# Kernel optimization log

Hardware: AMD Instinct MI355X
Metric: run time of the kernel (lower is better)

The kernel has to match this reference:

```python
import jax, jax.numpy as jnp
import numpy as np
import math

NUM_HEADS = 16
VEC_SIZE = 1024
HEAD_DIM = VEC_SIZE // NUM_HEADS


def setup_inputs() -> dict:
    key = jax.random.key(0)
    k1, k2, k3, k4, k5 = jax.random.split(key, 5)
    B, S, D = 2, 2048, VEC_SIZE
    x = jax.random.normal(k1, (B, S, D), dtype=jnp.float32)
    # Linear params, torch-style: y = x @ W.T + b
    s1 = 1.0 / math.sqrt(D)
    W_qkv = jax.random.uniform(k2, (3 * D, D), minval=-s1, maxval=s1, dtype=jnp.float32)
    b_qkv = jax.random.uniform(k3, (3 * D,), minval=-s1, maxval=s1, dtype=jnp.float32)
    W_out = jax.random.uniform(k4, (D, D), minval=-s1, maxval=s1, dtype=jnp.float32)
    b_out = jax.random.uniform(k5, (D,), minval=-s1, maxval=s1, dtype=jnp.float32)
    return {"x": x, "W_qkv": W_qkv, "b_qkv": b_qkv, "W_out": W_out, "b_out": b_out}


def reference(x, W_qkv, b_qkv, W_out, b_out):
    B, S, D = x.shape
    H, Hd = NUM_HEADS, HEAD_DIM
    qkv = x @ W_qkv.T + b_qkv                      # [B,S,3D]
    q, k, v = jnp.split(qkv, 3, axis=-1)
    # [B,S,H,Hd] -> [B,H,S,Hd]
    q = q.reshape(B, S, H, Hd).transpose(0, 2, 1, 3)
    k = k.reshape(B, S, H, Hd).transpose(0, 2, 1, 3)
    v = v.reshape(B, S, H, Hd).transpose(0, 2, 1, 3)
    weight = jnp.einsum('bhqd,bhkd->bhqk', q, k)   # [B,H,S,S]
    causal = jnp.triu(jnp.ones((S, S), dtype=bool), k=1)
    weight = jnp.where(causal, -jnp.inf, weight)
    weight = weight / jnp.sqrt(jnp.asarray(Hd, dtype=weight.dtype))
    weight = jax.nn.softmax(weight, axis=-1)
    out = jnp.einsum('bhqk,bhkd->bhqd', weight, v)  # [B,H,S,Hd]
    out = out.transpose(0, 2, 1, 3).reshape(B, S, D)
    return out @ W_out.T + b_out
```

## Files before the change

kernel.cpp:

```cpp
#include <hip/hip_runtime.h>
#include <hip/hip_bf16.h>

typedef __attribute__((ext_vector_type(8))) short short8;
typedef __attribute__((ext_vector_type(4))) short s4v;
typedef __attribute__((ext_vector_type(4))) float floatx4;

__device__ inline floatx4 mfma_bf16(short8 a, short8 b, floatx4 c) {
  return __builtin_amdgcn_mfma_f32_16x16x32_bf16(a, b, c, 0, 0, 0);
}
__device__ inline float exp2_fast(float x) { return __builtin_amdgcn_exp2f(x); }

__device__ inline short bf16s(float f) {
  __hip_bfloat16 h = __float2bfloat16(f);
  return *reinterpret_cast<short*>(&h);
}
__device__ inline float sbf16(short s) {
  return __bfloat162float(*reinterpret_cast<__hip_bfloat16*>(&s));
}

__device__ inline void gld16(__hip_bfloat16* lds, const __hip_bfloat16* g) {
  __builtin_amdgcn_global_load_lds(
      (const __attribute__((address_space(1))) void*)g,
      (__attribute__((address_space(3))) void*)lds, 16, 0, 0);
}

__global__ __launch_bounds__(256) void cvt_all(
    const float* __restrict__ x, const float* __restrict__ wqkv,
    const float* __restrict__ wout, __hip_bfloat16* __restrict__ xb,
    __hip_bfloat16* __restrict__ wqkvb, __hip_bfloat16* __restrict__ wob) {
  const int n1 = 4194304, n2 = 3145728;
  int i = (blockIdx.x * 256 + threadIdx.x) * 8;
  const float* src;
  __hip_bfloat16* dst;
  int off;
  if (i < n1) { src = x; dst = xb; off = i; }
  else if (i < n1 + n2) { src = wqkv; dst = wqkvb; off = i - n1; }
  else { src = wout; dst = wob; off = i - n1 - n2; }
  float4 a = *reinterpret_cast<const float4*>(src + off);
  float4 b = *reinterpret_cast<const float4*>(src + off + 4);
  __hip_bfloat16 t[8];
  t[0] = __float2bfloat16(a.x); t[1] = __float2bfloat16(a.y);
  t[2] = __float2bfloat16(a.z); t[3] = __float2bfloat16(a.w);
  t[4] = __float2bfloat16(b.x); t[5] = __float2bfloat16(b.y);
  t[6] = __float2bfloat16(b.z); t[7] = __float2bfloat16(b.w);
  *reinterpret_cast<short8*>(dst + off) = *reinterpret_cast<short8*>(t);
}

__device__ inline void stage_half(__hip_bfloat16* lds, const __hip_bfloat16* g,
                                  int K, int tid) {
#pragma unroll
  for (int it = 0; it < 2; ++it) {
    int idx = it * 512 + tid;
    int row = idx >> 3, col = ((idx & 7) ^ (row & 7)) * 8;
    gld16(lds + idx * 8, g + (size_t)row * K + col);
  }
}
__device__ inline void stage_q(__hip_bfloat16* lds, const __hip_bfloat16* g,
                               int K, int tid) {
  int row = tid >> 3, col = ((tid & 7) ^ (row & 7)) * 8;
  gld16(lds + tid * 8, g + (size_t)row * K + col);
}

#define VMW(N) asm volatile("s_waitcnt vmcnt(" #N ")" ::: "memory")
#define BAR __builtin_amdgcn_s_barrier()

#define LDA8(dst, BUF, MH)                                                     \
  do {                                                                         \
    _Pragma("unroll") for (int mf = 0; mf < 4; ++mf) {                         \
      int rh = wm * 64 + mf * 16 + l15;                                        \
      _Pragma("unroll") for (int ks = 0; ks < 2; ++ks)                         \
          dst[mf][ks] = *reinterpret_cast<const short8*>(                      \
              &SA[BUF][MH][rh * 64 + (((ks * 4 + quad) ^ (rh & 7)) * 8)]);     \
    }                                                                          \
  } while (0)
#define LDB4(dst, BUF, NH)                                                     \
  do {                                                                         \
    _Pragma("unroll") for (int nf = 0; nf < 2; ++nf) {                         \
      int rh = wn * 32 + nf * 16 + l15;                                        \
      _Pragma("unroll") for (int ks = 0; ks < 2; ++ks)                         \
          dst[nf][ks] = *reinterpret_cast<const short8*>(                      \
              &SB[BUF][NH][rh * 64 + (((ks * 4 + quad) ^ (rh & 7)) * 8)]);     \
    }                                                                          \
  } while (0)
#define MM16(MH, NH, AF, BF)                                                   \
  do {                                                                         \
    _Pragma("unroll") for (int mf = 0; mf < 4; ++mf)                           \
        _Pragma("unroll") for (int nf = 0; nf < 2; ++nf) {                     \
      acc[MH][NH][mf][nf] = mfma_bf16(AF[mf][0], BF[nf][0], acc[MH][NH][mf][nf]); \
      acc[MH][NH][mf][nf] = mfma_bf16(AF[mf][1], BF[nf][1], acc[MH][NH][mf][nf]); \
    }                                                                          \
  } while (0)
#define PH(RD, STG, MH, NH, AF, BF, WT)                                        \
  do {                                                                         \
    RD;                                                                        \
    STG;                                                                       \
    __builtin_amdgcn_s_setprio(1);                                             \
    MM16(MH, NH, AF, BF);                                                      \
    __builtin_amdgcn_s_setprio(0);                                             \
    WT;                                                                        \
    BAR;                                                                       \
  } while (0)

template<bool OUT_BF16>
__global__ __launch_bounds__(512, 2) void gemm_256(
    const __hip_bfloat16* __restrict__ A, const __hip_bfloat16* __restrict__ Bt,
    const float* __restrict__ bias, void* __restrict__ Cout,
    int M, int N, int K) {
  __shared__ __align__(16) __hip_bfloat16 SA[2][2][128 * 64];
  __shared__ __align__(16) __hip_bfloat16 SB[2][2][128 * 64];
  const int tid = threadIdx.x;
  const int lane = tid & 63, quad = (lane >> 4), l15 = lane & 15;
  const int wave = tid >> 6;
  const int wm = wave >> 2, wn = wave & 3;

  const int nbx = gridDim.x;
  int bid = blockIdx.y * nbx + blockIdx.x;
  const int nwg = nbx * gridDim.y;
  if ((nwg & 7) == 0) bid = (bid & 7) * (nwg >> 3) + (bid >> 3);
  const int bx = bid % nbx, by = bid / nbx;
  const int m0 = by * 256, n0 = bx * 256;

  const __hip_bfloat16* Abase = A + (size_t)m0 * K;
  const __hip_bfloat16* Bbase = Bt + (size_t)n0 * K;
  const int NT = K >> 6;

  floatx4 acc[2][2][4][2];
#pragma unroll
  for (int a = 0; a < 2; ++a)
#pragma unroll
    for (int b = 0; b < 2; ++b)
#pragma unroll
      for (int c = 0; c < 4; ++c)
#pragma unroll
        for (int d = 0; d < 2; ++d) acc[a][b][c][d] = (floatx4){0.f, 0.f, 0.f, 0.f};

  short8 af0[4][2], af1[4][2];
  short8 bf0[2][2], bf1[2][2];

  stage_half(&SA[0][0][0], Abase, K, tid);
  stage_half(&SB[0][0][0], Bbase, K, tid);
  stage_half(&SA[0][1][0], Abase + (size_t)128 * K, K, tid);
  stage_half(&SB[0][1][0], Bbase + (size_t)128 * K, K, tid);
  stage_half(&SA[1][0][0], Abase + 64, K, tid);
  stage_half(&SB[1][0][0], Bbase + 64, K, tid);
  stage_half(&SA[1][1][0], Abase + (size_t)128 * K + 64, K, tid);
  stage_half(&SB[1][1][0], Bbase + (size_t)128 * K + 64, K, tid);
  VMW(12);
  BAR;

  for (int t = 0; t <= NT - 3; ++t) {
    const int cb = t & 1;
    const size_t k2 = (size_t)(t + 2) * 64;
    PH({ LDA8(af0, cb, 0); LDB4(bf0, cb, 0); }, (void)0,
       0, 0, af0, bf0, VMW(10));
    PH(LDA8(af1, cb, 1),
       { stage_half(&SA[cb][0][0], Abase + k2, K, tid);
         stage_half(&SB[cb][0][0], Bbase + k2, K, tid); },
       1, 0, af1, bf0, VMW(12));
    PH(LDB4(bf1, cb, 1),
       stage_half(&SA[cb][1][0], Abase + (size_t)128 * K + k2, K, tid),
       1, 1, af1, bf1, (void)0);
    PH((void)0,
       stage_half(&SB[cb][1][0], Bbase + (size_t)128 * K + k2, K, tid),
       0, 1, af0, bf1, VMW(12));
  }
  {
    const int cb = (NT - 2) & 1;
    PH({ LDA8(af0, cb, 0); LDB4(bf0, cb, 0); }, (void)0, 0, 0, af0, bf0, VMW(10));
    PH(LDA8(af1, cb, 1), (void)0, 1, 0, af1, bf0, VMW(8));
    PH(LDB4(bf1, cb, 1), (void)0, 1, 1, af1, bf1, (void)0);
    PH((void)0, (void)0, 0, 1, af0, bf1, VMW(4));
  }
  {
    const int cb = (NT - 1) & 1;
    PH({ LDA8(af0, cb, 0); LDB4(bf0, cb, 0); }, (void)0, 0, 0, af0, bf0, VMW(2));
    PH(LDA8(af1, cb, 1), (void)0, 1, 0, af1, bf0, VMW(0));
    LDB4(bf1, cb, 1);
    __builtin_amdgcn_s_setprio(1);
    MM16(1, 1, af1, bf1);
    MM16(0, 1, af0, bf1);
    __builtin_amdgcn_s_setprio(0);
  }

#pragma unroll
  for (int nh = 0; nh < 2; ++nh)
#pragma unroll
    for (int nf = 0; nf < 2; ++nf) {
      int gn = n0 + nh * 128 + wn * 32 + nf * 16 + l15;
      float bv = bias[gn];
#pragma unroll
      for (int mh = 0; mh < 2; ++mh)
#pragma unroll
        for (int mf = 0; mf < 4; ++mf)
#pragma unroll
          for (int rg = 0; rg < 4; ++rg) {
            int gm = m0 + mh * 128 + wm * 64 + mf * 16 + quad * 4 + rg;
            float v = acc[mh][nh][mf][nf][rg] + bv;
            if (OUT_BF16)
              ((__hip_bfloat16*)Cout)[(size_t)gm * N + gn] = __float2bfloat16(v);
            else
              ((float*)Cout)[(size_t)gm * N + gn] = v;
          }
    }
}

__global__ __launch_bounds__(512, 2) void gemm_n64(
    const __hip_bfloat16* __restrict__ A, const __hip_bfloat16* __restrict__ Bt,
    const float* __restrict__ bias, float* __restrict__ Cout,
    int M, int N, int K) {
  __shared__ __align__(16) __hip_bfloat16 SA[3][2][128 * 64];
  __shared__ __align__(16) __hip_bfloat16 SB[3][64 * 64];
  const int tid = threadIdx.x;
  const int lane = tid & 63, quad = (lane >> 4), l15 = lane & 15;
  const int wave = tid >> 6;
  const int wm = wave >> 2, wn = wave & 3;

  const int nbx = gridDim.x;
  int bid = blockIdx.y * nbx + blockIdx.x;
  const int nwg = nbx * gridDim.y;
  if ((nwg & 7) == 0) bid = (bid & 7) * (nwg >> 3) + (bid >> 3);
  const int bx = bid % nbx, by = bid / nbx;
  const int m0 = by * 256, n0 = bx * 64;

  const __hip_bfloat16* Abase = A + (size_t)m0 * K;
  const __hip_bfloat16* Bbase = Bt + (size_t)n0 * K;
  const int NT = K >> 6;

  floatx4 acc[2][4];
#pragma unroll
  for (int a = 0; a < 2; ++a)
#pragma unroll
    for (int c = 0; c < 4; ++c) acc[a][c] = (floatx4){0.f, 0.f, 0.f, 0.f};

  short8 af0[4][2], af1[4][2];
  short8 bf[2];

#define N64_LDA(dst, BUF, MH)                                                  \
  do {                                                                         \
    _Pragma("unroll") for (int mf = 0; mf < 4; ++mf) {                         \
      int rh = wm * 64 + mf * 16 + l15;                                        \
      _Pragma("unroll") for (int ks = 0; ks < 2; ++ks)                         \
          dst[mf][ks] = *reinterpret_cast<const short8*>(                      \
              &SA[BUF][MH][rh * 64 + (((ks * 4 + quad) ^ (rh & 7)) * 8)]);     \
    }                                                                          \
  } while (0)
#define N64_LDB(BUF)                                                           \
  do {                                                                         \
    int rh = wn * 16 + l15;                                                    \
    _Pragma("unroll") for (int ks = 0; ks < 2; ++ks)                           \
        bf[ks] = *reinterpret_cast<const short8*>(                             \
            &SB[BUF][rh * 64 + (((ks * 4 + quad) ^ (rh & 7)) * 8)]);           \
  } while (0)
#define N64_MM(MH, AF)                                                         \
  do {                                                                         \
    _Pragma("unroll") for (int mf = 0; mf < 4; ++mf) {                         \
      acc[MH][mf] = mfma_bf16(AF[mf][0], bf[0], acc[MH][mf]);                  \
      acc[MH][mf] = mfma_bf16(AF[mf][1], bf[1], acc[MH][mf]);                  \
    }                                                                          \
  } while (0)

  stage_half(&SA[0][0][0], Abase, K, tid);
  stage_half(&SA[0][1][0], Abase + (size_t)128 * K, K, tid);
  stage_q(&SB[0][0], Bbase, K, tid);
  stage_half(&SA[1][0][0], Abase + 64, K, tid);
  stage_half(&SA[1][1][0], Abase + (size_t)128 * K + 64, K, tid);
  stage_q(&SB[1][0], Bbase + 64, K, tid);
  VMW(5);
  BAR;

  int cb = 0, sb = 2;
  for (int t = 0; t <= NT - 3; ++t) {
    const size_t k2 = (size_t)(t + 2) * 64;
    N64_LDA(af0, cb, 0);
    N64_LDA(af1, cb, 1);
    N64_LDB(cb);
    stage_half(&SA[sb][0][0], Abase + k2, K, tid);
    stage_half(&SA[sb][1][0], Abase + (size_t)128 * K + k2, K, tid);
    stage_q(&SB[sb][0], Bbase + k2, K, tid);
    __builtin_amdgcn_s_setprio(1);
    N64_MM(0, af0);
    N64_MM(1, af1);
    __builtin_amdgcn_s_setprio(0);
    VMW(5);
    BAR;
    cb = (cb == 2) ? 0 : cb + 1;
    sb = (sb == 2) ? 0 : sb + 1;
  }
  {
    N64_LDA(af0, cb, 0);
    N64_LDA(af1, cb, 1);
    N64_LDB(cb);
    __builtin_amdgcn_s_setprio(1);
    N64_MM(0, af0);
    N64_MM(1, af1);
    __builtin_amdgcn_s_setprio(0);
    VMW(0);
    BAR;
    cb = (cb == 2) ? 0 : cb + 1;
  }
  {
    N64_LDA(af0, cb, 0);
    N64_LDA(af1, cb, 1);
    N64_LDB(cb);
    __builtin_amdgcn_s_setprio(1);
    N64_MM(0, af0);
    N64_MM(1, af1);
    __builtin_amdgcn_s_setprio(0);
  }

  {
    int gn = n0 + wn * 16 + l15;
    float bv = bias[gn];
#pragma unroll
    for (int mh = 0; mh < 2; ++mh)
#pragma unroll
      for (int mf = 0; mf < 4; ++mf)
#pragma unroll
        for (int rg = 0; rg < 4; ++rg) {
          int gm = m0 + mh * 128 + wm * 64 + mf * 16 + quad * 4 + rg;
          Cout[(size_t)gm * N + gn] = acc[mh][mf][rg] + bv;
        }
  }
#undef N64_LDA
#undef N64_LDB
#undef N64_MM
}

__global__ __launch_bounds__(256, 3) void flash_attn(
    const __hip_bfloat16* __restrict__ qkv, __hip_bfloat16* __restrict__ out) {
  const int S = 2048, QKV = 3072;
  const int bx = blockIdx.x;
  const int g = (blockIdx.y >> 3) + 2 * blockIdx.z;
  int qt;
  if (g == 0)      qt = bx;
  else if (g == 1) qt = 31 - bx;
  else if (g == 2) qt = (bx + 8) & 31;
  else             qt = (23 - bx) & 31;
  const int h = blockIdx.y, b = blockIdx.z;
  const int q0 = qt * 64;
  __shared__ __align__(16) short Ps[2][64 * 64];
  const int tid = threadIdx.x;
  const int wave = tid >> 6, lane = tid & 63, quad = lane >> 4, l15 = lane & 15;
  const int rx = l15 & 7;
  const __hip_bfloat16* base = qkv + (size_t)b * S * QKV;
  const float c2 = 0.18033688011112042f;
  const floatx4 zero4 = {0.f, 0.f, 0.f, 0.f};
  const int krow = 16 * wave + l15;

  const __hip_bfloat16* kbase = base + 1024 + h * 64;
  const __hip_bfloat16* vbase = base + 2048 + h * 64;

  for (int it = 0; it < 2; ++it) {
    int v = tid + it * 256;
    int row = v >> 3, cb = v & 7;
    int colp = (cb ^ (row & 7)) * 8;
    short8 qv = *reinterpret_cast<const short8*>(
        base + (size_t)(q0 + row) * QKV + h * 64 + cb * 8);
    short qs[8];
    for (int e = 0; e < 8; ++e) qs[e] = bf16s(sbf16(qv[e]) * c2);
    *reinterpret_cast<short8*>(&Ps[1][row * 64 + colp]) = *reinterpret_cast<short8*>(qs);
  }
  short8 kA0 = *reinterpret_cast<const short8*>(
      kbase + (size_t)krow * QKV + quad * 8);
  short8 kA1 = *reinterpret_cast<const short8*>(
      kbase + (size_t)krow * QKV + 32 + quad * 8);
  __syncthreads();

  short8 aq[4][2];
  for (int t4 = 0; t4 < 4; ++t4)
    for (int s = 0; s < 2; ++s)
      aq[t4][s] = *reinterpret_cast<const short8*>(
          &Ps[1][(t4 * 16 + l15) * 64 + (((s * 4 + quad) ^ rx) * 8)]);

  floatx4 o_acc[4];
  for (int m = 0; m < 4; ++m) o_acc[m] = zero4;
  float lsum4[4] = {0.f, 0.f, 0.f, 0.f};
  short8 vA0, vA1;

  for (int j = 0; j <= qt; ++j) {
    const int cj = j & 1, pj = cj ^ 1;

    short8 kB0, kB1, vB0, vB1;
    if (j < qt) {
      const __hip_bfloat16* kp = kbase + (size_t)((j + 1) * 64 + krow) * QKV;
      kB0 = *reinterpret_cast<const short8*>(kp + quad * 8);
      kB1 = *reinterpret_cast<const short8*>(kp + 32 + quad * 8);
    }
    {
      const __hip_bfloat16* vp = vbase + (size_t)(j * 64 + quad * 8) * QKV + krow;
      for (int i = 0; i < 8; ++i) {
        vB0[i] = *reinterpret_cast<const short*>(vp + (size_t)i * QKV);
        vB1[i] = *reinterpret_cast<const short*>(vp + (size_t)(32 + i) * QKV);
      }
    }

    if (j > 0) {
      for (int s = 0; s < 2; ++s) {
        short8 bv = s ? vA1 : vA0;
        for (int m = 0; m < 4; ++m) {
          short8 ap = *reinterpret_cast<const short8*>(
              &Ps[pj][(m * 16 + l15) * 64 + (((4 * s + quad) ^ rx) * 8)]);
          o_acc[m] = mfma_bf16(ap, bv, o_acc[m]);
        }
      }
    }

    floatx4 sc[4];
    for (int t4 = 0; t4 < 4; ++t4) {
      sc[t4] = mfma_bf16(kA0, aq[t4][0], zero4);
      sc[t4] = mfma_bf16(kA1, aq[t4][1], sc[t4]);
    }
    if (j == qt) {
      int kloc = 16 * wave + quad * 4;
      for (int t4 = 0; t4 < 4; ++t4)
        for (int rg = 0; rg < 4; ++rg)
          if (kloc + rg > t4 * 16 + l15) sc[t4][rg] = -1e30f;
    }

    const int pcol = ((2 * wave + (quad >> 1)) ^ rx) * 8 + (quad & 1) * 4;
    for (int t4 = 0; t4 < 4; ++t4) {
      short pp[4];
      for (int rg = 0; rg < 4; ++rg) {
        float p = exp2_fast(sc[t4][rg]);
        lsum4[t4] += p;
        pp[rg] = bf16s(p);
      }
      *reinterpret_cast<s4v*>(&Ps[cj][(t4 * 16 + l15) * 64 + pcol]) =
          *reinterpret_cast<s4v*>(pp);
    }

    kA0 = kB0; kA1 = kB1; vA0 = vB0; vA1 = vB1;
    __syncthreads();
  }

  const int pq = qt & 1;
  for (int s = 0; s < 2; ++s) {
    short8 bv = s ? vA1 : vA0;
    for (int m = 0; m < 4; ++m) {
      short8 ap = *reinterpret_cast<const short8*>(
          &Ps[pq][(m * 16 + l15) * 64 + (((4 * s + quad) ^ rx) * 8)]);
      o_acc[m] = mfma_bf16(ap, bv, o_acc[m]);
    }
  }
  for (int t4 = 0; t4 < 4; ++t4) {
    lsum4[t4] += __shfl_xor(lsum4[t4], 16);
    lsum4[t4] += __shfl_xor(lsum4[t4], 32);
  }
  float* Lf = (float*)&Ps[pq ^ 1][0];
  if (quad == 0)
    for (int t4 = 0; t4 < 4; ++t4)
      Lf[wave * 64 + t4 * 16 + l15] = lsum4[t4];
  __syncthreads();
  if (tid < 64)
    Lf[256 + tid] = 1.0f / (Lf[tid] + Lf[64 + tid] + Lf[128 + tid] + Lf[192 + tid]);
  __syncthreads();

  const int dcol = h * 64 + krow;
  for (int m = 0; m < 4; ++m)
    for (int rg = 0; rg < 4; ++rg) {
      int q = m * 16 + quad * 4 + rg;
      out[(size_t)(b * S + q0 + q) * 1024 + dcol] =
          __float2bfloat16(o_acc[m][rg] * Lf[256 + q]);
    }
}

extern "C" void kernel_launch(void* const* d_in, const int* in_sizes, int n_in,
                              void* d_out, int out_size, void* d_ws, size_t ws_size,
                              hipStream_t stream) {
  const float* x    = (const float*)d_in[0];
  const float* Wqkv = (const float*)d_in[1];
  const float* bqkv = (const float*)d_in[2];
  const float* Wout = (const float*)d_in[3];
  const float* bout = (const float*)d_in[4];
  float* out = (float*)d_out;

  const int BS = 2 * 2048;
  const int D = 1024;
  char* ws = (char*)d_ws;
  __hip_bfloat16* xb    = (__hip_bfloat16*)(ws);
  __hip_bfloat16* wqkvb = (__hip_bfloat16*)(ws + (size_t)8  * 1048576);
  __hip_bfloat16* wob   = (__hip_bfloat16*)(ws + (size_t)14 * 1048576);
  __hip_bfloat16* qkvb  = (__hip_bfloat16*)(ws + (size_t)16 * 1048576);
  __hip_bfloat16* attnb = (__hip_bfloat16*)(ws + (size_t)40 * 1048576);

  cvt_all<<<4096, 256, 0, stream>>>(x, Wqkv, Wout, xb, wqkvb, wob);

  gemm_256<true><<<dim3(3072 / 256, BS / 256), 512, 0, stream>>>(
      xb, wqkvb, bqkv, qkvb, BS, 3 * D, D);

  flash_attn<<<dim3(32, 16, 2), 256, 0, stream>>>(qkvb, attnb);

  gemm_n64<<<dim3(1024 / 64, BS / 256), 512, 0, stream>>>(
      attnb, wob, bout, out, BS, D, D);
}
```

Baseline: 168.2 us.

## Software-pipeline GEMM LDS fragment loads across k-tiles and raise attention occupancy

Restructures the 256x256 GEMM main loop so the A/B fragments for the next k-tile are read from LDS during the last MFMA phase of the current tile. It double-buffers the af0 registers and unrolls the loop by two so buffer indices become constants. This is meant to hide LDS read latency behind MFMA work and drop one barrier-bound phase per tile. It also raises flash_attn launch bounds from 3 to 4 blocks per SM, which may force register spills. The extra fragment registers could likewise pressure the GEMM's 2-block occupancy, and the loop now assumes NT is even.

```diff
diff --git a/kernel.cpp b/kernel.cpp
--- a/kernel.cpp
+++ b/kernel.cpp
@@ -90,15 +90,31 @@
       acc[MH][NH][mf][nf] = mfma_bf16(AF[mf][1], BF[nf][1], acc[MH][NH][mf][nf]); \
     }                                                                          \
   } while (0)
-#define PH(RD, STG, MH, NH, AF, BF, WT)                                        \
-  do {                                                                         \
-    RD;                                                                        \
-    STG;                                                                       \
+#define TILE6(CB, NB, AF0C, AF0N, STG1, STG2, STG3, W0, W2, W3)                \
+  do {                                                                         \
+    LDA8(af1, CB, 1);                                                          \
     __builtin_amdgcn_s_setprio(1);                                             \
-    MM16(MH, NH, AF, BF);                                                      \
+    MM16(0, 0, AF0C, bf0);                                                     \
     __builtin_amdgcn_s_setprio(0);                                             \
-    WT;                                                                        \
+    W0; BAR;                                                                   \
+    LDB4(bf1, CB, 1);                                                          \
+    STG1;                                                                      \
+    __builtin_amdgcn_s_setprio(1);                                             \
+    MM16(1, 0, af1, bf0);                                                      \
+    __builtin_amdgcn_s_setprio(0);                                             \
     BAR;                                                                       \
+    STG2;                                                                      \
+    __builtin_amdgcn_s_setprio(1);                                             \
+    MM16(1, 1, af1, bf1);                                                      \
+    __builtin_amdgcn_s_setprio(0);                                             \
+    W2; BAR;                                                                   \
+    LDA8(AF0N, NB, 0);                                                         \
+    LDB4(bf0, NB, 0);                                                          \
+    STG3;                                                                      \
+    __builtin_amdgcn_s_setprio(1);                                             \
+    MM16(0, 1, AF0C, bf1);                                                     \
+    __builtin_amdgcn_s_setprio(0);                                             \
+    W3; BAR;                                                                   \
   } while (0)
 
 template<bool OUT_BF16>
@@ -134,7 +150,8 @@
 #pragma unroll
         for (int d = 0; d < 2; ++d) acc[a][b][c][d] = (floatx4){0.f, 0.f, 0.f, 0.f};
 
-  short8 af0[4][2], af1[4][2];
+  short8 af0A[4][2], af0B[4][2];
+  short8 af1[4][2];
   short8 bf0[2][2], bf1[2][2];
 
   stage_half(&SA[0][0][0], Abase, K, tid);
@@ -147,38 +164,44 @@
   stage_half(&SB[1][1][0], Bbase + (size_t)128 * K + 64, K, tid);
   VMW(12);
   BAR;
-
-  for (int t = 0; t <= NT - 3; ++t) {
-    const int cb = t & 1;
-    const size_t k2 = (size_t)(t + 2) * 64;
-    PH({ LDA8(af0, cb, 0); LDB4(bf0, cb, 0); }, (void)0,
-       0, 0, af0, bf0, VMW(10));
-    PH(LDA8(af1, cb, 1),
-       { stage_half(&SA[cb][0][0], Abase + k2, K, tid);
-         stage_half(&SB[cb][0][0], Bbase + k2, K, tid); },
-       1, 0, af1, bf0, VMW(12));
-    PH(LDB4(bf1, cb, 1),
-       stage_half(&SA[cb][1][0], Abase + (size_t)128 * K + k2, K, tid),
-       1, 1, af1, bf1, (void)0);
-    PH((void)0,
-       stage_half(&SB[cb][1][0], Bbase + (size_t)128 * K + k2, K, tid),
-       0, 1, af0, bf1, VMW(12));
+  LDA8(af0A, 0, 0);
+  LDB4(bf0, 0, 0);
+  VMW(10);
+  BAR;
+
+  for (int t = 0; t <= NT - 4; t += 2) {
+    const size_t k2 = (size_t)(t + 2) * 64, k3 = (size_t)(t + 3) * 64;
+    TILE6(0, 1, af0A, af0B,
+          { stage_half(&SA[0][0][0], Abase + k2, K, tid);
+            stage_half(&SB[0][0][0], Bbase + k2, K, tid); },
+          stage_half(&SA[0][1][0], Abase + (size_t)128 * K + k2, K, tid),
+          stage_half(&SB[0][1][0], Bbase + (size_t)128 * K + k2, K, tid),
+          VMW(8), VMW(10), VMW(10));
+    TILE6(1, 0, af0B, af0A,
+          { stage_half(&SA[1][0][0], Abase + k3, K, tid);
+            stage_half(&SB[1][0][0], Bbase + k3, K, tid); },
+          stage_half(&SA[1][1][0], Abase + (size_t)128 * K + k3, K, tid),
+          stage_half(&SB[1][1][0], Bbase + (size_t)128 * K + k3, K, tid),
+          VMW(8), VMW(10), VMW(10));
   }
   {
-    const int cb = (NT - 2) & 1;
-    PH({ LDA8(af0, cb, 0); LDB4(bf0, cb, 0); }, (void)0, 0, 0, af0, bf0, VMW(10));
-    PH(LDA8(af1, cb, 1), (void)0, 1, 0, af1, bf0, VMW(8));
-    PH(LDB4(bf1, cb, 1), (void)0, 1, 1, af1, bf1, (void)0);
-    PH((void)0, (void)0, 0, 1, af0, bf1, VMW(4));
+    TILE6(0, 1, af0A, af0B, (void)0, (void)0, (void)0, VMW(8), VMW(4), VMW(2));
   }
   {
-    const int cb = (NT - 1) & 1;
-    PH({ LDA8(af0, cb, 0); LDB4(bf0, cb, 0); }, (void)0, 0, 0, af0, bf0, VMW(2));
-    PH(LDA8(af1, cb, 1), (void)0, 1, 0, af1, bf0, VMW(0));
-    LDB4(bf1, cb, 1);
+    LDA8(af1, 1, 1);
+    __builtin_amdgcn_s_setprio(1);
+    MM16(0, 0, af0B, bf0);
+    __builtin_amdgcn_s_setprio(0);
+    VMW(0);
+    BAR;
+    LDB4(bf1, 1, 1);
+    __builtin_amdgcn_s_setprio(1);
+    MM16(1, 0, af1, bf0);
+    __builtin_amdgcn_s_setprio(0);
+    BAR;
     __builtin_amdgcn_s_setprio(1);
     MM16(1, 1, af1, bf1);
-    MM16(0, 1, af0, bf1);
+    MM16(0, 1, af0B, bf1);
     __builtin_amdgcn_s_setprio(0);
   }
 
@@ -326,7 +349,7 @@
 #undef N64_MM
 }
 
-__global__ __launch_bounds__(256, 3) void flash_attn(
+__global__ __launch_bounds__(256, 4) void flash_attn(
     const __hip_bfloat16* __restrict__ qkv, __hip_bfloat16* __restrict__ out) {
   const int S = 2048, QKV = 3072;
   const int bx = blockIdx.x;
```

New measurement: 226.6 us. 1.35x slower.

## Retile output projection GEMM to 128x64 blocks with 256 threads

Applied to the files above, without the earlier changes.

The output-projection GEMM moves from 256x64 tiles on 512-thread blocks to 128x64 tiles on 256-thread blocks, with each of 4 waves computing a 64x32 sub-tile. This doubles the grid to 512 workgroups so the CUs are better filled on a small 4096x1024 GEMM, and it raises per-wave MFMA reuse of B fragments. In exchange, each block reuses B over fewer rows, so total global and LDS traffic for B rises. The LDS footprint per block also shrinks.

```diff
diff --git a/kernel.cpp b/kernel.cpp
--- a/kernel.cpp
+++ b/kernel.cpp
@@ -55,10 +55,23 @@
     gld16(lds + idx * 8, g + (size_t)row * K + col);
   }
 }
-__device__ inline void stage_q(__hip_bfloat16* lds, const __hip_bfloat16* g,
-                               int K, int tid) {
-  int row = tid >> 3, col = ((tid & 7) ^ (row & 7)) * 8;
-  gld16(lds + tid * 8, g + (size_t)row * K + col);
+__device__ inline void stage_a128_t256(__hip_bfloat16* lds, const __hip_bfloat16* g,
+                                       int K, int tid) {
+#pragma unroll
+  for (int it = 0; it < 4; ++it) {
+    int idx = it * 256 + tid;
+    int row = idx >> 3, col = ((idx & 7) ^ (row & 7)) * 8;
+    gld16(lds + idx * 8, g + (size_t)row * K + col);
+  }
+}
+__device__ inline void stage_b64_t256(__hip_bfloat16* lds, const __hip_bfloat16* g,
+                                      int K, int tid) {
+#pragma unroll
+  for (int it = 0; it < 2; ++it) {
+    int idx = it * 256 + tid;
+    int row = idx >> 3, col = ((idx & 7) ^ (row & 7)) * 8;
+    gld16(lds + idx * 8, g + (size_t)row * K + col);
+  }
 }
 
 #define VMW(N) asm volatile("s_waitcnt vmcnt(" #N ")" ::: "memory")
@@ -204,126 +217,109 @@
     }
 }
 
-__global__ __launch_bounds__(512, 2) void gemm_n64(
+__global__ __launch_bounds__(256, 2) void gemm_n64b(
     const __hip_bfloat16* __restrict__ A, const __hip_bfloat16* __restrict__ Bt,
     const float* __restrict__ bias, float* __restrict__ Cout,
     int M, int N, int K) {
-  __shared__ __align__(16) __hip_bfloat16 SA[3][2][128 * 64];
+  __shared__ __align__(16) __hip_bfloat16 SA[3][128 * 64];
   __shared__ __align__(16) __hip_bfloat16 SB[3][64 * 64];
   const int tid = threadIdx.x;
-  const int lane = tid & 63, quad = (lane >> 4), l15 = lane & 15;
-  const int wave = tid >> 6;
-  const int wm = wave >> 2, wn = wave & 3;
+  const int wave = tid >> 6, lane = tid & 63, quad = lane >> 4, l15 = lane & 15;
+  const int wm = (wave >> 1) * 64, wn = (wave & 1) * 32;
 
   const int nbx = gridDim.x;
   int bid = blockIdx.y * nbx + blockIdx.x;
   const int nwg = nbx * gridDim.y;
   if ((nwg & 7) == 0) bid = (bid & 7) * (nwg >> 3) + (bid >> 3);
   const int bx = bid % nbx, by = bid / nbx;
-  const int m0 = by * 256, n0 = bx * 64;
+  const int m0 = by * 128, n0 = bx * 64;
 
   const __hip_bfloat16* Abase = A + (size_t)m0 * K;
   const __hip_bfloat16* Bbase = Bt + (size_t)n0 * K;
   const int NT = K >> 6;
 
-  floatx4 acc[2][4];
-#pragma unroll
-  for (int a = 0; a < 2; ++a)
-#pragma unroll
-    for (int c = 0; c < 4; ++c) acc[a][c] = (floatx4){0.f, 0.f, 0.f, 0.f};
-
-  short8 af0[4][2], af1[4][2];
-  short8 bf[2];
-
-#define N64_LDA(dst, BUF, MH)                                                  \
-  do {                                                                         \
-    _Pragma("unroll") for (int mf = 0; mf < 4; ++mf) {                         \
-      int rh = wm * 64 + mf * 16 + l15;                                        \
+  floatx4 acc[4][2];
+#pragma unroll
+  for (int r = 0; r < 4; ++r)
+#pragma unroll
+    for (int c = 0; c < 2; ++c) acc[r][c] = (floatx4){0.f, 0.f, 0.f, 0.f};
+
+  short8 af[4][2], bf[2][2];
+
+#define NB_RD(BUF)                                                             \
+  do {                                                                         \
+    _Pragma("unroll") for (int r = 0; r < 4; ++r) {                            \
+      int row = wm + r * 16 + l15;                                             \
       _Pragma("unroll") for (int ks = 0; ks < 2; ++ks)                         \
-          dst[mf][ks] = *reinterpret_cast<const short8*>(                      \
-              &SA[BUF][MH][rh * 64 + (((ks * 4 + quad) ^ (rh & 7)) * 8)]);     \
+          af[r][ks] = *reinterpret_cast<const short8*>(                        \
+              &SA[BUF][row * 64 + (((ks * 4 + quad) ^ (l15 & 7)) * 8)]);       \
     }                                                                          \
-  } while (0)
-#define N64_LDB(BUF)                                                           \
-  do {                                                                         \
-    int rh = wn * 16 + l15;                                                    \
+    _Pragma("unroll") for (int c = 0; c < 2; ++c) {                            \
+      int row = wn + c * 16 + l15;                                             \
+      _Pragma("unroll") for (int ks = 0; ks < 2; ++ks)                         \
+          bf[c][ks] = *reinterpret_cast<const short8*>(                        \
+              &SB[BUF][row * 64 + (((ks * 4 + quad) ^ (l15 & 7)) * 8)]);       \
+    }                                                                          \
+  } while (0)
+#define NB_MM                                                                  \
+  do {                                                                         \
     _Pragma("unroll") for (int ks = 0; ks < 2; ++ks)                           \
-        bf[ks] = *reinterpret_cast<const short8*>(                             \
-            &SB[BUF][rh * 64 + (((ks * 4 + quad) ^ (rh & 7)) * 8)]);           \
-  } while (0)
-#define N64_MM(MH, AF)                                                         \
-  do {                                                                         \
-    _Pragma("unroll") for (int mf = 0; mf < 4; ++mf) {                         \
-      acc[MH][mf] = mfma_bf16(AF[mf][0], bf[0], acc[MH][mf]);                  \
-      acc[MH][mf] = mfma_bf16(AF[mf][1], bf[1], acc[MH][mf]);                  \
-    }                                                                          \
-  } while (0)
-
-  stage_half(&SA[0][0][0], Abase, K, tid);
-  stage_half(&SA[0][1][0], Abase + (size_t)128 * K, K, tid);
-  stage_q(&SB[0][0], Bbase, K, tid);
-  stage_half(&SA[1][0][0], Abase + 64, K, tid);
-  stage_half(&SA[1][1][0], Abase + (size_t)128 * K + 64, K, tid);
-  stage_q(&SB[1][0], Bbase + 64, K, tid);
-  VMW(5);
+        _Pragma("unroll") for (int r = 0; r < 4; ++r)                          \
+            _Pragma("unroll") for (int c = 0; c < 2; ++c)                      \
+                acc[r][c] = mfma_bf16(af[r][ks], bf[c][ks], acc[r][c]);        \
+  } while (0)
+
+  stage_a128_t256(&SA[0][0], Abase, K, tid);
+  stage_b64_t256(&SB[0][0], Bbase, K, tid);
+  stage_a128_t256(&SA[1][0], Abase + 64, K, tid);
+  stage_b64_t256(&SB[1][0], Bbase + 64, K, tid);
+  VMW(6);
   BAR;
 
   int cb = 0, sb = 2;
   for (int t = 0; t <= NT - 3; ++t) {
     const size_t k2 = (size_t)(t + 2) * 64;
-    N64_LDA(af0, cb, 0);
-    N64_LDA(af1, cb, 1);
-    N64_LDB(cb);
-    stage_half(&SA[sb][0][0], Abase + k2, K, tid);
-    stage_half(&SA[sb][1][0], Abase + (size_t)128 * K + k2, K, tid);
-    stage_q(&SB[sb][0], Bbase + k2, K, tid);
+    NB_RD(cb);
+    stage_a128_t256(&SA[sb][0], Abase + k2, K, tid);
+    stage_b64_t256(&SB[sb][0], Bbase + k2, K, tid);
     __builtin_amdgcn_s_setprio(1);
-    N64_MM(0, af0);
-    N64_MM(1, af1);
+    NB_MM;
     __builtin_amdgcn_s_setprio(0);
-    VMW(5);
+    VMW(6);
     BAR;
     cb = (cb == 2) ? 0 : cb + 1;
     sb = (sb == 2) ? 0 : sb + 1;
   }
   {
-    N64_LDA(af0, cb, 0);
-    N64_LDA(af1, cb, 1);
-    N64_LDB(cb);
+    NB_RD(cb);
     __builtin_amdgcn_s_setprio(1);
-    N64_MM(0, af0);
-    N64_MM(1, af1);
+    NB_MM;
     __builtin_amdgcn_s_setprio(0);
     VMW(0);
     BAR;
     cb = (cb == 2) ? 0 : cb + 1;
   }
   {
-    N64_LDA(af0, cb, 0);
-    N64_LDA(af1, cb, 1);
-    N64_LDB(cb);
+    NB_RD(cb);
     __builtin_amdgcn_s_setprio(1);
-    N64_MM(0, af0);
-    N64_MM(1, af1);
+    NB_MM;
     __builtin_amdgcn_s_setprio(0);
   }
 
-  {
-    int gn = n0 + wn * 16 + l15;
+#pragma unroll
+  for (int c = 0; c < 2; ++c) {
+    int gn = n0 + wn + c * 16 + l15;
     float bv = bias[gn];
 #pragma unroll
-    for (int mh = 0; mh < 2; ++mh)
-#pragma unroll
-      for (int mf = 0; mf < 4; ++mf)
-#pragma unroll
-        for (int rg = 0; rg < 4; ++rg) {
-          int gm = m0 + mh * 128 + wm * 64 + mf * 16 + quad * 4 + rg;
-          Cout[(size_t)gm * N + gn] = acc[mh][mf][rg] + bv;
-        }
-  }
-#undef N64_LDA
-#undef N64_LDB
-#undef N64_MM
+    for (int r = 0; r < 4; ++r)
+#pragma unroll
+      for (int rg = 0; rg < 4; ++rg) {
+        int gm = m0 + wm + r * 16 + quad * 4 + rg;
+        Cout[(size_t)gm * N + gn] = acc[r][c][rg] + bv;
+      }
+  }
+#undef NB_RD
+#undef NB_MM
 }
 
 __global__ __launch_bounds__(256, 3) void flash_attn(
@@ -490,6 +486,6 @@
 
   flash_attn<<<dim3(32, 16, 2), 256, 0, stream>>>(qkvb, attnb);
 
-  gemm_n64<<<dim3(1024 / 64, BS / 256), 512, 0, stream>>>(
+  gemm_n64b<<<dim3(1024 / 64, BS / 128), 256, 0, stream>>>(
       attnb, wob, bout, out, BS, D, D);
 }
```

Result: no change. 165.3 us (-1.7%).
